# Kernel optimization log

Hardware: AMD Instinct MI355X
Metric: run time of the kernel (lower is better)

## Reference

```python
import jax, jax.numpy as jnp
import numpy as np

EMB_DIM = 1024
NUM_HEADS = 16
HEAD_DIM = EMB_DIM // NUM_HEADS
B, S = 4, 1024


def _split_heads(x):
    # [B, S, E] -> [B, H, S, E/H]
    b, s, e = x.shape
    return x.reshape(b, s, NUM_HEADS, e // NUM_HEADS).transpose(0, 2, 1, 3)


def _merge_heads(x):
    # [B, H, S, D] -> [B, S, H*D]
    b, h, s, d = x.shape
    return x.transpose(0, 2, 1, 3).reshape(b, s, h * d)


def setup_inputs() -> dict:
    key = jax.random.key(0)
    ks = jax.random.split(key, 8)
    w_scale = 0.02
    return {
        "Re": jax.random.normal(ks[0], (B, S, EMB_DIM), jnp.float32),
        "Im": jax.random.normal(ks[1], (B, S, EMB_DIM), jnp.float32),
        "pos_enc": jax.random.normal(ks[2], (B, S, HEAD_DIM), jnp.float32),
        "Wq": jax.random.normal(ks[3], (EMB_DIM, EMB_DIM), jnp.float32) * w_scale,
        "bq": jnp.zeros((EMB_DIM,), jnp.float32),
        "Wk": jax.random.normal(ks[4], (EMB_DIM, EMB_DIM), jnp.float32) * w_scale,
        "bk": jnp.zeros((EMB_DIM,), jnp.float32),
        "Wv": jax.random.normal(ks[5], (EMB_DIM, EMB_DIM), jnp.float32) * w_scale,
        "bv": jnp.zeros((EMB_DIM,), jnp.float32),
        "Wo": jax.random.normal(ks[6], (EMB_DIM, EMB_DIM), jnp.float32) * w_scale,
        "bo": jnp.zeros((EMB_DIM,), jnp.float32),
    }


def reference(Re, Im, pos_enc, Wq, bq, Wk, bk, Wv, bv, Wo, bo):
    # projections + head split
    Q = _split_heads(Re @ Wq + bq)          # [B,H,S,D]
    K = _split_heads(Re @ Wk + bk)          # [B,H,S,D]
    ImH = _split_heads(Im)                  # [B,H,S,D]
    P = pos_enc[:, None, :, :]              # [B,1,S,D] broadcast over heads
    Q = Q + P
    K = K + P
    # real part of (Q + i*Im)(K - i*Im)^T = Q K^T + Im Im^T
    denom = jnp.sqrt(jnp.asarray(EMB_DIM, Q.dtype))  # NOTE: sqrt(emb_dim), as in source
    scores = (jnp.einsum("bhqd,bhkd->bhqk", Q, K)
              + jnp.einsum("bhqd,bhkd->bhqk", ImH, ImH)) / denom
    weights = jax.nn.softmax(scores, axis=-1)
    V = _split_heads(Re @ Wv + bv) + P      # value_pos_enc=True
    out = jnp.einsum("bhqk,bhkd->bhqd", weights, V)
    return _merge_heads(out) @ Wo + bo
```

## Files before the change

### kernel.cpp

```cpp
#include <hip/hip_runtime.h>
#include <hip/hip_bf16.h>
#include <stdint.h>

#define BATCH 4
#define SEQ   1024
#define EMB   1024
#define NHEAD 16
#define HDIM  64
#define MTOT  (BATCH*SEQ)
#define MELEM (MTOT*EMB)

typedef __attribute__((ext_vector_type(8))) short short8;
typedef __attribute__((ext_vector_type(4))) float f32x4;
typedef __attribute__((ext_vector_type(16))) float f32x16;
typedef __attribute__((ext_vector_type(4))) unsigned short us4;
typedef __attribute__((ext_vector_type(2))) unsigned int u32x2;
typedef __attribute__((ext_vector_type(4))) unsigned int u32x4;

#define WAITV(N) asm volatile("s_waitcnt vmcnt(" #N ")" ::: "memory")
#define BARRIER() __builtin_amdgcn_s_barrier()

static __device__ __forceinline__ unsigned short f2bf_fast(float f) {
  unsigned u = __builtin_bit_cast(unsigned, f);
  return (unsigned short)((u + 0x8000u) >> 16);
}

static __device__ __forceinline__ unsigned cvt_pk_bf16(float lo, float hi) {
  unsigned r;
  asm("v_cvt_pk_bf16_f32 %0, %1, %2" : "=v"(r) : "v"(lo), "v"(hi));
  return r;
}

static __device__ __forceinline__ void cp16(const void* g, const void* lds_uniform) {
  __builtin_amdgcn_global_load_lds(
      (const __attribute__((address_space(1))) unsigned int*)(uintptr_t)g,
      (__attribute__((address_space(3))) unsigned int*)(unsigned int)(uintptr_t)lds_uniform,
      16, 0, 0);
}

__global__ __launch_bounds__(256) void prep(const float* __restrict__ Re,
                                            const float* __restrict__ Im,
                                            short* __restrict__ Rebf,
                                            short* __restrict__ Imbf,
                                            const float* __restrict__ W0,
                                            const float* __restrict__ W1,
                                            const float* __restrict__ W2,
                                            const float* __restrict__ W3,
                                            short* __restrict__ WtBase) {
  __shared__ short tile[32][33];
  const int bid = blockIdx.x;
  if (bid < 8192) {
    const float* in  = (bid >= 4096) ? Im   : Re;
    short*       out = (bid >= 4096) ? Imbf : Rebf;
    int i = (bid & 4095) * 256 + threadIdx.x;
    float4 f = ((const float4*)in)[i];
    unsigned r0 = ((unsigned)f2bf_fast(f.y) << 16) | f2bf_fast(f.x);
    unsigned r1 = ((unsigned)f2bf_fast(f.w) << 16) | f2bf_fast(f.z);
    ((uint2*)out)[i] = make_uint2(r0, r1);
  } else {
    const int wb = bid - 8192;
    const int z = wb >> 10;
    const float* W = (z == 0) ? W0 : (z == 1) ? W1 : (z == 2) ? W2 : W3;
    short* Wt = WtBase + (size_t)z * EMB * EMB;
    const int rem = wb & 1023;
    const int nT = (rem & 31) * 32, kT = (rem >> 5) * 32;
    const int tx = threadIdx.x & 31, ty = threadIdx.x >> 5;
    #pragma unroll
    for (int i = 0; i < 4; ++i)
      tile[ty + 8*i][tx] = (short)f2bf_fast(W[(size_t)(kT + ty + 8*i) * EMB + nT + tx]);
    __syncthreads();
    #pragma unroll
    for (int i = 0; i < 4; ++i)
      Wt[(size_t)(nT + ty + 8*i) * EMB + kT + tx] = tile[tx][ty + 8*i];
  }
}

__global__ __launch_bounds__(256) void gemm_qkv(const short* __restrict__ A,
                                                const short* __restrict__ Wt,
                                                const float* __restrict__ bq,
                                                const float* __restrict__ bk,
                                                const float* __restrict__ bv,
                                                const float* __restrict__ pos,
                                                short* __restrict__ QKbase,
                                                short* __restrict__ vtOut) {
  const int m0 = blockIdx.y * 128, n0 = blockIdx.x * 128;
  const int z = n0 >> 10;
  const float* bias = (z == 0) ? bq : (z == 1 ? bk : bv);

  __shared__ __align__(16) short As[2][128 * 64];
  __shared__ __align__(16) short Bs[2][128 * 64];

  const int t = threadIdx.x;
  const int lane = t & 63, w = t >> 6;
  const int wm = w >> 1, wn = w & 1;
  const int quad = lane >> 4, l16 = lane & 15;
  const int lrow8 = lane >> 3, lchunk = lane & 7;
  const int gch = lchunk ^ lrow8;
  const int sw7 = l16 & 7;

  const short* Arow = A  + (size_t)(m0 + w * 32 + lrow8) * EMB + gch * 8;
  const short* Brow = Wt + (size_t)(n0 + w * 32 + lrow8) * EMB + gch * 8;

  f32x4 acc[4][4] = {};

  auto STAGE = [&](short* as, short* bs, int k0) {
    #pragma unroll
    for (int s = 0; s < 4; ++s)
      cp16(Arow + (size_t)(s * 8) * EMB + k0, &as[(w * 32 + s * 8) * 64]);
    #pragma unroll
    for (int s = 0; s < 4; ++s)
      cp16(Brow + (size_t)(s * 8) * EMB + k0, &bs[(w * 32 + s * 8) * 64]);
  };
  auto COMPUTE = [&](const short* as, const short* bs) {
    #pragma unroll
    for (int ks = 0; ks < 2; ++ks) {
      const int chv = ((ks << 2) + quad) ^ sw7;
      short8 af[4], bfr[4];
      #pragma unroll
      for (int i = 0; i < 4; ++i)
        af[i] = *(const short8*)&as[(wm * 64 + i * 16 + l16) * 64 + chv * 8];
      #pragma unroll
      for (int j = 0; j < 4; ++j)
        bfr[j] = *(const short8*)&bs[(wn * 64 + j * 16 + l16) * 64 + chv * 8];
      #pragma unroll
      for (int i = 0; i < 4; ++i)
        #pragma unroll
        for (int j = 0; j < 4; ++j)
          acc[i][j] = __builtin_amdgcn_mfma_f32_16x16x32_bf16(af[i], bfr[j], acc[i][j], 0, 0, 0);
    }
  };

  STAGE(As[0], Bs[0], 0);
  STAGE(As[1], Bs[1], 64);

  #pragma unroll 1
  for (int p = 0; p < 7; ++p) {
    WAITV(8); BARRIER();
    COMPUTE(As[0], Bs[0]);
    BARRIER();
    STAGE(As[0], Bs[0], p * 128 + 128);
    WAITV(8); BARRIER();
    COMPUTE(As[1], Bs[1]);
    BARRIER();
    STAGE(As[1], Bs[1], p * 128 + 192);
  }
  WAITV(8); BARRIER();
  COMPUTE(As[0], Bs[0]);
  BARRIER();
  WAITV(0); BARRIER();
  COMPUTE(As[1], Bs[1]);

  #pragma unroll
  for (int i = 0; i < 4; ++i) {
    int mbase = m0 + wm * 64 + i * 16 + quad * 4;
    #pragma unroll
    for (int j = 0; j < 4; ++j) {
      int n = n0 + wn * 64 + j * 16 + l16;
      int nl = n & 1023;
      float bn = bias[nl];
      int d = nl & (HDIM - 1);
      if (z == 2) {
        int bh = (mbase >> 10) * NHEAD + (nl >> 6);
        int s = mbase & (SEQ - 1);
        us4 pk;
        #pragma unroll
        for (int r = 0; r < 4; ++r) {
          float v = acc[i][j][r] + bn + pos[(size_t)(mbase + r) * HDIM + d];
          pk[r] = f2bf_fast(v);
        }
        *(us4*)&vtOut[((size_t)bh * HDIM + d) * SEQ + s] = pk;
      } else {
        #pragma unroll
        for (int r = 0; r < 4; ++r) {
          int mm = mbase + r;
          float v = acc[i][j][r] + bn + pos[(size_t)mm * HDIM + d];
          QKbase[(size_t)z * MELEM + (size_t)mm * EMB + nl] = (short)f2bf_fast(v);
        }
      }
    }
  }
}

__global__ __launch_bounds__(256) void gemm_wo(const short* __restrict__ A,
                                               const short* __restrict__ Bt,
                                               const float* __restrict__ bias,
                                               float* __restrict__ out) {
  const int m0 = blockIdx.y * 64, n0 = blockIdx.x * 64;

  __shared__ __align__(16) short As[2][64 * 64];
  __shared__ __align__(16) short Bs[2][64 * 64];

  const int t = threadIdx.x;
  const int lane = t & 63, w = t >> 6;
  const int wm = w >> 1, wn = w & 1;
  const int quad = lane >> 4, l16 = lane & 15;
  const int lrow8 = lane >> 3, lchunk = lane & 7;
  const int gch = lchunk ^ lrow8;
  const int sw7 = l16 & 7;

  const short* Arow = A  + (size_t)(m0 + w * 16 + lrow8) * EMB + gch * 8;
  const short* Brow = Bt + (size_t)(n0 + w * 16 + lrow8) * EMB + gch * 8;

  f32x4 acc[2][2] = {};

  auto STAGE = [&](short* as, short* bs, int k0) {
    #pragma unroll
    for (int s = 0; s < 2; ++s) {
      cp16(Arow + (size_t)(s * 8) * EMB + k0, &as[(w * 16 + s * 8) * 64]);
      cp16(Brow + (size_t)(s * 8) * EMB + k0, &bs[(w * 16 + s * 8) * 64]);
    }
  };
  auto COMPUTE = [&](const short* as, const short* bs) {
    #pragma unroll
    for (int ks = 0; ks < 2; ++ks) {
      const int chv = ((ks << 2) + quad) ^ sw7;
      short8 af[2], bfr[2];
      #pragma unroll
      for (int i = 0; i < 2; ++i)
        af[i] = *(const short8*)&as[(wm * 32 + i * 16 + l16) * 64 + chv * 8];
      #pragma unroll
      for (int j = 0; j < 2; ++j)
        bfr[j] = *(const short8*)&bs[(wn * 32 + j * 16 + l16) * 64 + chv * 8];
      #pragma unroll
      for (int i = 0; i < 2; ++i)
        #pragma unroll
        for (int j = 0; j < 2; ++j)
          acc[i][j] = __builtin_amdgcn_mfma_f32_16x16x32_bf16(af[i], bfr[j], acc[i][j], 0, 0, 0);
    }
  };

  STAGE(As[0], Bs[0], 0);
  STAGE(As[1], Bs[1], 64);

  #pragma unroll 1
  for (int p = 0; p < 7; ++p) {
    WAITV(4); BARRIER();
    COMPUTE(As[0], Bs[0]);
    BARRIER();
    STAGE(As[0], Bs[0], p * 128 + 128);
    WAITV(4); BARRIER();
    COMPUTE(As[1], Bs[1]);
    BARRIER();
    STAGE(As[1], Bs[1], p * 128 + 192);
  }
  WAITV(4); BARRIER();
  COMPUTE(As[0], Bs[0]);
  BARRIER();
  WAITV(0); BARRIER();
  COMPUTE(As[1], Bs[1]);

  #pragma unroll
  for (int i = 0; i < 2; ++i) {
    int mbase = m0 + wm * 32 + i * 16 + quad * 4;
    #pragma unroll
    for (int j = 0; j < 2; ++j) {
      int n = n0 + wn * 32 + j * 16 + l16;
      float bn = bias[n];
      #pragma unroll
      for (int r = 0; r < 4; ++r)
        out[(size_t)(mbase + r) * EMB + n] = acc[i][j][r] + bn;
    }
  }
}

__global__ __launch_bounds__(256) void attn(const short* __restrict__ Qp,
                                            const short* __restrict__ Kp,
                                            const short* __restrict__ VtG,
                                            const short* __restrict__ Imb,
                                            short* __restrict__ attnA) {
  const int qb = blockIdx.y * 128;
  const int bh = blockIdx.x;
  const int b = bh >> 4, h = bh & 15;
  const int t = threadIdx.x, lane = t & 63, w = t >> 6;
  const int c31 = lane & 31;
  const int hi  = lane >> 5;
  const int lrow8 = lane >> 3, lchunk = lane & 7;
  const int gch = lchunk ^ lrow8;

  __shared__ __align__(16) short tiles[3 * 64 * 64];

  const int qrow = qb + w * 32 + c31;
  const size_t qbase = ((size_t)(b * SEQ + qrow)) * EMB + h * HDIM + hi * 8;
  short8 bq_[4], bim[4];
  #pragma unroll
  for (int ks = 0; ks < 4; ++ks) {
    bq_[ks] = *(const short8*)&Qp [qbase + ks * 16];
    bim[ks] = *(const short8*)&Imb[qbase + ks * 16];
  }

  float lrA = 0.f, lrB = 0.f;
  f32x16 o0 = {}, o1 = {};

  const float SC = 0.03125f * 1.44269504089f;
  const size_t kimBase = ((size_t)b * SEQ) * EMB + h * HDIM + gch * 8;
  const size_t vtBase  = ((size_t)bh * HDIM) * SEQ + gch * 8;

  #pragma unroll
  for (int s = 0; s < 6; ++s) {
    const int I = w * 6 + s;
    const int tz = I >> 3;
    const int row = ((I & 7) * 8) + lrow8;
    const short* g;
    if (tz == 0)      g = Kp  + kimBase + (size_t)row * EMB;
    else if (tz == 1) g = Imb + kimBase + (size_t)row * EMB;
    else              g = VtG + vtBase + (size_t)row * SEQ;
    cp16(g, &tiles[I * 512]);
  }
  __syncthreads();

  const int swz = c31 & 7;

  for (int kt = 0; kt < 16; ++kt) {
    const int kBaseN = (kt + 1) * 64;

    f32x16 s0 = {}, s1 = {};
    #pragma unroll
    for (int ks = 0; ks < 4; ++ks) {
      const int ch = ((ks * 2 + hi) ^ swz) * 8;
      const int r0off = c31 * 64 + ch, r1off = (32 + c31) * 64 + ch;
      short8 k0 = *(const short8*)&tiles[r0off];
      short8 k1 = *(const short8*)&tiles[r1off];
      short8 i0 = *(const short8*)&tiles[4096 + r0off];
      short8 i1 = *(const short8*)&tiles[4096 + r1off];
      s0 = __builtin_amdgcn_mfma_f32_32x32x16_bf16(k0, bq_[ks], s0, 0, 0, 0);
      s1 = __builtin_amdgcn_mfma_f32_32x32x16_bf16(k1, bq_[ks], s1, 0, 0, 0);
      s0 = __builtin_amdgcn_mfma_f32_32x32x16_bf16(i0, bim[ks], s0, 0, 0, 0);
      s1 = __builtin_amdgcn_mfma_f32_32x32x16_bf16(i1, bim[ks], s1, 0, 0, 0);
    }

    __syncthreads();

    if (kt != 15) {
      #pragma unroll
      for (int s = 0; s < 4; ++s) {
        const int I = w * 4 + s;
        const int row = ((I & 7) * 8) + lrow8;
        const short* g = ((I >> 3) ? Imb : Kp) + kimBase + (size_t)(kBaseN + row) * EMB;
        cp16(g, &tiles[I * 512]);
      }
    }

    float p0[16], p1[16];
    #pragma unroll
    for (int r = 0; r < 16; ++r) {
      p0[r] = __builtin_amdgcn_exp2f(s0[r] * SC);
      p1[r] = __builtin_amdgcn_exp2f(s1[r] * SC);
      lrA += p0[r];
      lrB += p1[r];
    }

    short8 ap[4];
    #pragma unroll
    for (int half = 0; half < 2; ++half) {
      {
        u32x2 sA = __builtin_amdgcn_permlane32_swap(
            cvt_pk_bf16(p0[half*8+0], p0[half*8+1]), cvt_pk_bf16(p0[half*8+4], p0[half*8+5]), false, false);
        u32x2 sB = __builtin_amdgcn_permlane32_swap(
            cvt_pk_bf16(p0[half*8+2], p0[half*8+3]), cvt_pk_bf16(p0[half*8+6], p0[half*8+7]), false, false);
        u32x4 wv = {sA[0], sB[0], sA[1], sB[1]};
        ap[half] = __builtin_bit_cast(short8, wv);
      }
      {
        u32x2 sA = __builtin_amdgcn_permlane32_swap(
            cvt_pk_bf16(p1[half*8+0], p1[half*8+1]), cvt_pk_bf16(p1[half*8+4], p1[half*8+5]), false, false);
        u32x2 sB = __builtin_amdgcn_permlane32_swap(
            cvt_pk_bf16(p1[half*8+2], p1[half*8+3]), cvt_pk_bf16(p1[half*8+6], p1[half*8+7]), false, false);
        u32x4 wv = {sA[0], sB[0], sA[1], sB[1]};
        ap[2 + half] = __builtin_bit_cast(short8, wv);
      }
    }

    #pragma unroll
    for (int ks = 0; ks < 4; ++ks) {
      const int ch = ((ks * 2 + hi) ^ swz) * 8;
      short8 v0 = *(const short8*)&tiles[8192 + c31 * 64 + ch];
      short8 v1 = *(const short8*)&tiles[8192 + (32 + c31) * 64 + ch];
      o0 = __builtin_amdgcn_mfma_f32_32x32x16_bf16(ap[ks], v0, o0, 0, 0, 0);
      o1 = __builtin_amdgcn_mfma_f32_32x32x16_bf16(ap[ks], v1, o1, 0, 0, 0);
    }

    __syncthreads();

    if (kt != 15) {
      #pragma unroll
      for (int s = 0; s < 2; ++s) {
        const int I = 16 + w * 2 + s;
        const int row = ((I & 7) * 8) + lrow8;
        cp16(VtG + vtBase + (size_t)row * SEQ + kBaseN, &tiles[I * 512]);
      }
    }
  }

  float lr = lrA + lrB;
  lr += __shfl_xor(lr, 32);
  float inv = 1.f / lr;

  #pragma unroll
  for (int r = 0; r < 16; ++r) {
    const int qr = (r & 3) + 8 * (r >> 2) + 4 * hi;
    const float invr = __shfl(inv, qr);
    const size_t base = ((size_t)(b * SEQ + qb + w * 32 + qr)) * EMB + h * HDIM + c31;
    attnA[base]      = (short)f2bf_fast(o0[r] * invr);
    attnA[base + 32] = (short)f2bf_fast(o1[r] * invr);
  }
}

extern "C" void kernel_launch(void* const* d_in, const int* in_sizes, int n_in,
                              void* d_out, int out_size, void* d_ws, size_t ws_size,
                              hipStream_t stream) {
  const float* Re  = (const float*)d_in[0];
  const float* Im  = (const float*)d_in[1];
  const float* pos = (const float*)d_in[2];
  const float* Wq  = (const float*)d_in[3];
  const float* bq  = (const float*)d_in[4];
  const float* Wk  = (const float*)d_in[5];
  const float* bk  = (const float*)d_in[6];
  const float* Wv  = (const float*)d_in[7];
  const float* bv  = (const float*)d_in[8];
  const float* Wo  = (const float*)d_in[9];
  const float* bo  = (const float*)d_in[10];

  short* ws    = (short*)d_ws;
  short* Rebf  = ws;
  short* Imbf  = ws + (size_t)MELEM;
  short* Wt    = ws + (size_t)2 * MELEM;
  short* Qp    = ws + (size_t)3 * MELEM;
  short* Kp    = Qp + (size_t)MELEM;
  short* VtG   = Qp + (size_t)2 * MELEM;
  short* attnA = ws + (size_t)6 * MELEM;

  prep<<<dim3(12288), 256, 0, stream>>>(Re, Im, Rebf, Imbf, Wq, Wk, Wv, Wo, Wt);

  gemm_qkv<<<dim3(3 * EMB / 128, MTOT / 128), 256, 0, stream>>>(
      Rebf, Wt, bq, bk, bv, pos, Qp, VtG);

  attn<<<dim3(BATCH * NHEAD, SEQ / 128), 256, 0, stream>>>(
      Qp, Kp, VtG, Imbf, attnA);

  gemm_wo<<<dim3(EMB / 64, MTOT / 64), 256, 0, stream>>>(
      attnA, Wt + 3 * EMB * EMB, bo, (float*)d_out);
}
```

Before: 190.2 us.

## Double-buffer attention K/Im/V tiles in LDS with two-ahead prefetch

Splits the single shared-memory tile set into two buffers. Each iteration loads the K, Im and V^T tiles two steps ahead and waits with a vmcnt count, so one barrier-fenced phase replaces the two mid-iteration syncs and staggered reloads. It also raises wave priority around the MFMA blocks with s_setprio. The cost is twice the LDS per block, which could limit how many blocks fit on a CU, and a more fragile wait-count scheme.

```diff
diff --git a/kernel.cpp b/kernel.cpp
--- a/kernel.cpp
+++ b/kernel.cpp
@@ -277,7 +277,7 @@
   const int lrow8 = lane >> 3, lchunk = lane & 7;
   const int gch = lchunk ^ lrow8;
 
-  __shared__ __align__(16) short tiles[3 * 64 * 64];
+  __shared__ __align__(16) short tiles[2][3 * 64 * 64];
 
   const int qrow = qb + w * 32 + c31;
   const size_t qbase = ((size_t)(b * SEQ + qrow)) * EMB + h * HDIM + hi * 8;
@@ -295,50 +295,39 @@
   const size_t kimBase = ((size_t)b * SEQ) * EMB + h * HDIM + gch * 8;
   const size_t vtBase  = ((size_t)bh * HDIM) * SEQ + gch * 8;
 
-  #pragma unroll
-  for (int s = 0; s < 6; ++s) {
-    const int I = w * 6 + s;
-    const int tz = I >> 3;
-    const int row = ((I & 7) * 8) + lrow8;
-    const short* g;
-    if (tz == 0)      g = Kp  + kimBase + (size_t)row * EMB;
-    else if (tz == 1) g = Imb + kimBase + (size_t)row * EMB;
-    else              g = VtG + vtBase + (size_t)row * SEQ;
-    cp16(g, &tiles[I * 512]);
-  }
-  __syncthreads();
+  auto STAGE_SET = [&](int ktile, short* buf) {
+    #pragma unroll
+    for (int s = 0; s < 6; ++s) {
+      const int I = w * 6 + s;
+      const int tz = I >> 3;
+      const int row = ((I & 7) * 8) + lrow8;
+      const short* g;
+      if (tz == 0)      g = Kp  + kimBase + (size_t)(ktile * 64 + row) * EMB;
+      else if (tz == 1) g = Imb + kimBase + (size_t)(ktile * 64 + row) * EMB;
+      else              g = VtG + vtBase + (size_t)row * SEQ + ktile * 64;
+      cp16(g, &buf[I * 512]);
+    }
+  };
 
   const int swz = c31 & 7;
 
-  for (int kt = 0; kt < 16; ++kt) {
-    const int kBaseN = (kt + 1) * 64;
-
+  auto PHASE = [&](const short* cur) {
     f32x16 s0 = {}, s1 = {};
+    __builtin_amdgcn_s_setprio(1);
     #pragma unroll
     for (int ks = 0; ks < 4; ++ks) {
       const int ch = ((ks * 2 + hi) ^ swz) * 8;
       const int r0off = c31 * 64 + ch, r1off = (32 + c31) * 64 + ch;
-      short8 k0 = *(const short8*)&tiles[r0off];
-      short8 k1 = *(const short8*)&tiles[r1off];
-      short8 i0 = *(const short8*)&tiles[4096 + r0off];
-      short8 i1 = *(const short8*)&tiles[4096 + r1off];
+      short8 k0 = *(const short8*)&cur[r0off];
+      short8 k1 = *(const short8*)&cur[r1off];
+      short8 i0 = *(const short8*)&cur[4096 + r0off];
+      short8 i1 = *(const short8*)&cur[4096 + r1off];
       s0 = __builtin_amdgcn_mfma_f32_32x32x16_bf16(k0, bq_[ks], s0, 0, 0, 0);
       s1 = __builtin_amdgcn_mfma_f32_32x32x16_bf16(k1, bq_[ks], s1, 0, 0, 0);
       s0 = __builtin_amdgcn_mfma_f32_32x32x16_bf16(i0, bim[ks], s0, 0, 0, 0);
       s1 = __builtin_amdgcn_mfma_f32_32x32x16_bf16(i1, bim[ks], s1, 0, 0, 0);
     }
-
-    __syncthreads();
-
-    if (kt != 15) {
-      #pragma unroll
-      for (int s = 0; s < 4; ++s) {
-        const int I = w * 4 + s;
-        const int row = ((I & 7) * 8) + lrow8;
-        const short* g = ((I >> 3) ? Imb : Kp) + kimBase + (size_t)(kBaseN + row) * EMB;
-        cp16(g, &tiles[I * 512]);
-      }
-    }
+    __builtin_amdgcn_s_setprio(0);
 
     float p0[16], p1[16];
     #pragma unroll
@@ -370,26 +359,32 @@
       }
     }
 
+    __builtin_amdgcn_s_setprio(1);
     #pragma unroll
     for (int ks = 0; ks < 4; ++ks) {
       const int ch = ((ks * 2 + hi) ^ swz) * 8;
-      short8 v0 = *(const short8*)&tiles[8192 + c31 * 64 + ch];
-      short8 v1 = *(const short8*)&tiles[8192 + (32 + c31) * 64 + ch];
+      short8 v0 = *(const short8*)&cur[8192 + c31 * 64 + ch];
+      short8 v1 = *(const short8*)&cur[8192 + (32 + c31) * 64 + ch];
       o0 = __builtin_amdgcn_mfma_f32_32x32x16_bf16(ap[ks], v0, o0, 0, 0, 0);
       o1 = __builtin_amdgcn_mfma_f32_32x32x16_bf16(ap[ks], v1, o1, 0, 0, 0);
     }
-
-    __syncthreads();
-
-    if (kt != 15) {
-      #pragma unroll
-      for (int s = 0; s < 2; ++s) {
-        const int I = 16 + w * 2 + s;
-        const int row = ((I & 7) * 8) + lrow8;
-        cp16(VtG + vtBase + (size_t)row * SEQ + kBaseN, &tiles[I * 512]);
-      }
-    }
-  }
+    __builtin_amdgcn_s_setprio(0);
+  };
+
+  STAGE_SET(0, tiles[0]);
+  STAGE_SET(1, tiles[1]);
+
+  #pragma unroll 1
+  for (int kt = 0; kt < 15; ++kt) {
+    WAITV(6); BARRIER();
+    const short* cur = tiles[kt & 1];
+    PHASE(cur);
+    BARRIER();
+    if (kt <= 13)
+      STAGE_SET(kt + 2, tiles[kt & 1]);
+  }
+  WAITV(0); BARRIER();
+  PHASE(tiles[1]);
 
   float lr = lrA + lrB;
   lr += __shfl_xor(lr, 32);
```

After: 195.3 us. +2.7%, slower.
